# Kernel optimization log

Hardware: AMD Instinct MI355X
Metric: run time of the kernel (lower is better)

Reference implementation:

```python
import math
import jax, jax.numpy as jnp
import numpy as np

B, S, D, H = 2, 2048, 2048, 16
HD = D // H  # 128
EPS = 1e-5


def setup_inputs() -> dict:
    key = jax.random.key(0)
    ks = jax.random.split(key, 7)
    x = jax.random.normal(ks[0], (B, S, D), jnp.float32)
    # RoPE tables: (seqlen, head_dim//2)
    theta = 10000.0
    inv_freq = 1.0 / (theta ** (np.arange(0, HD, 2, dtype=np.float32) / HD))
    t = np.arange(S, dtype=np.float32)
    freqs = np.outer(t, inv_freq)  # (S, HD//2)
    freqs_cos = jnp.asarray(np.cos(freqs), jnp.float32)
    freqs_sin = jnp.asarray(np.sin(freqs), jnp.float32)
    sc = 0.02
    wq = jax.random.normal(ks[1], (D, D), jnp.float32) * sc  # stored (in, out)
    wk = jax.random.normal(ks[2], (D, D), jnp.float32) * sc
    wv = jax.random.normal(ks[3], (D, D), jnp.float32) * sc
    wu = jax.random.normal(ks[4], (D, D), jnp.float32) * sc
    wo = jax.random.normal(ks[5], (D, D), jnp.float32) * sc
    norm_w = jnp.ones((D,), jnp.float32)
    return {"x": x, "freqs_cos": freqs_cos, "freqs_sin": freqs_sin,
            "wq": wq, "wk": wk, "wv": wv, "wu": wu, "wo": wo, "norm_w": norm_w}


def _rope(t, cos, sin):
    # t: (B, S, H, HD); cos/sin: (S, HD//2)
    tr = t.reshape(t.shape[:-1] + (-1, 2))
    r, i = tr[..., 0], tr[..., 1]
    c = cos[None, :, None, :]
    s = sin[None, :, None, :]
    out_r = r * c - i * s
    out_i = r * s + i * c
    return jnp.stack([out_r, out_i], axis=-1).reshape(t.shape)


def reference(x, freqs_cos, freqs_sin, wq, wk, wv, wu, wo, norm_w):
    b, s, d = x.shape
    h = jax.nn.silu(x)  # pre-projection SiLU on the input
    q = (h @ wq).reshape(b, s, H, HD)
    k = (h @ wk).reshape(b, s, H, HD)
    v = (h @ wv).reshape(b, s, H, HD)
    u = h @ wu  # reshape->transpose->flatten in original is identity on (b,s,d)
    q = _rope(q, freqs_cos, freqs_sin)
    k = _rope(k, freqs_cos, freqs_sin)
    # scores: (b, H, s, s)
    scores = jnp.einsum('bqhd,bkhd->bhqk', q, k) / math.sqrt(HD)
    causal = jnp.tril(jnp.ones((s, s), bool))  # mask!=0 positions zeroed; silu(0)=0
    scores = jnp.where(causal[None, None], jax.nn.silu(scores), 0.0)
    out = jnp.einsum('bhqk,bkhd->bqhd', scores, v).reshape(b, s, d)
    # RMSNorm
    out = out * jax.lax.rsqrt(jnp.mean(out * out, axis=-1, keepdims=True) + EPS)
    out = out * norm_w
    out = out * u
    return out @ wo
```

## Files before the change

### kernel.cpp

```cpp
#include <hip/hip_runtime.h>
#include <hip/hip_bf16.h>
#include <cstdint>

typedef __attribute__((ext_vector_type(8))) short bf16x8;
typedef __attribute__((ext_vector_type(4))) float f32x4;
typedef unsigned short u16;

constexpr int B = 2, S = 2048, D = 2048, H = 16, HD = 128;
constexpr int M = B * S;
constexpr int NQKU = 6144;
constexpr float SCALE = 0.08838834764831845f;

static __device__ __forceinline__ float b2f(u16 u) {
    union { float f; uint32_t i; } v; v.i = ((uint32_t)u) << 16; return v.f;
}
static __device__ __forceinline__ u16 f2b(float f) {
    union { float f; uint32_t i; } v; v.f = f;
    uint32_t x = v.i;
    return (u16)((x + 0x7FFFu + ((x >> 16) & 1u)) >> 16);
}

__device__ __forceinline__ void gll16(const void* g, void* l) {
    __builtin_amdgcn_global_load_lds(
        (const __attribute__((address_space(1))) uint32_t*)g,
        (__attribute__((address_space(3))) uint32_t*)l, 16, 0, 0);
}

#define BAR() do { asm volatile("" ::: "memory"); __builtin_amdgcn_s_barrier(); \
                   asm volatile("" ::: "memory"); } while (0)

__global__ __launch_bounds__(256) void silu_cast(const float* __restrict__ x,
                                                 u16* __restrict__ h, int n) {
    int i = (blockIdx.x * 256 + threadIdx.x) * 4;
    if (i >= n) return;
    float4 v = *(const float4*)(x + i);
    ushort4 o;
    o.x = f2b(v.x / (1.f + __expf(-v.x)));
    o.y = f2b(v.y / (1.f + __expf(-v.y)));
    o.z = f2b(v.z / (1.f + __expf(-v.z)));
    o.w = f2b(v.w / (1.f + __expf(-v.w)));
    *(ushort4*)(h + i) = o;
}

__global__ __launch_bounds__(256) void wcast(const float* __restrict__ w,
                                             u16* __restrict__ wT) {
    __shared__ float t[64][65];
    int tx = threadIdx.x & 63, ty = threadIdx.x >> 6;
    int kb = blockIdx.y * 64, nb = blockIdx.x * 64;
    for (int r = ty; r < 64; r += 4)
        t[r][tx] = w[(size_t)(kb + r) * D + nb + tx];
    __syncthreads();
    for (int r = ty; r < 64; r += 4)
        wT[(size_t)(nb + r) * D + kb + tx] = f2b(t[tx][r]);
}

__global__ __launch_bounds__(512, 2)
void gemm_qkuv(const u16* __restrict__ A, const u16* __restrict__ BT,
               u16* __restrict__ qku, u16* __restrict__ vt) {
    __shared__ u16 lds[65536];
    const int tid = threadIdx.x;
    const int lane = tid & 63, wid = tid >> 6;
    const int wm = wid >> 2, wn = wid & 3;
    const int l16 = lane & 15, lq = lane >> 4;

    const int orig = blockIdx.x;
    const int swz = (orig & 7) * 64 + (orig >> 3);
    const int mt = swz & 15, nt = swz >> 4;
    const int m0 = mt * 256, n0 = nt * 256;

    const int srow = tid >> 2;
    const int ce = ((tid & 3) * 8) ^ (((tid >> 5) & 1) << 4);
    const int rdx = (lq * 16) ^ (((l16 >> 3) & 1) << 5);

    const u16* As0 = A + (size_t)(m0 + srow) * D + ce;
    const u16* Bs0 = BT + (size_t)(n0 + srow) * D + ce;

    {
        u16* dA = lds + wid * 512;
        u16* dB = lds + 16384 + wid * 512;
        gll16(As0,                    dA);
        gll16(As0 + (size_t)128 * D,  dA + 8192);
        gll16(Bs0,                    dB);
        gll16(Bs0 + (size_t)128 * D,  dB + 8192);
        gll16(As0 + 32,                    dA + 4096);
        gll16(As0 + 32 + (size_t)128 * D,  dA + 8192 + 4096);
        gll16(Bs0 + 32,                    dB + 4096);
        gll16(Bs0 + 32 + (size_t)128 * D,  dB + 8192 + 4096);
        u16* dA1 = lds + 32768 + wid * 512;
        u16* dB1 = lds + 32768 + 16384 + wid * 512;
        gll16(As0 + 64,                    dA1);
        gll16(As0 + 64 + (size_t)128 * D,  dA1 + 8192);
        gll16(Bs0 + 64,                    dB1);
        gll16(Bs0 + 64 + (size_t)128 * D,  dB1 + 8192);
    }
    asm volatile("s_waitcnt vmcnt(8)" ::: "memory");
    BAR();

    f32x4 acc[8][4] = {};
    bf16x8 a[8];
    const int rbB = (wn & 1) * 4096;

#define LOAD_A(kk)                                                            \
    _Pragma("unroll") for (int mi = 0; mi < 8; ++mi)                          \
        a[mi] = *(const bf16x8*)(Abase + (kk) * 8192 +                        \
                                 (mi * 16 + l16) * 64 + rdx);
#define LOAD_B(dst, nia, kk)                                                  \
    dst = *(const bf16x8*)(Bbase + (kk) * 8192 + rbB +                        \
                           ((nia) * 16 + l16) * 64 + rdx);
#define MFMA2(n0i, n1i)                                                       \
    __builtin_amdgcn_s_setprio(1);                                            \
    _Pragma("unroll") for (int mi = 0; mi < 8; ++mi) {                        \
        acc[mi][n0i] = __builtin_amdgcn_mfma_f32_16x16x32_bf16(a[mi], b0,     \
                            acc[mi][n0i], 0, 0, 0);                           \
        acc[mi][n1i] = __builtin_amdgcn_mfma_f32_16x16x32_bf16(a[mi], b1,     \
                            acc[mi][n1i], 0, 0, 0);                           \
    }                                                                          \
    __builtin_amdgcn_s_setprio(0);

    for (int kt = 0; kt < 32; ++kt) {
        const int buf = kt & 1;
        const char* Abase = (const char*)lds + buf * 65536 + wm * 16384;
        const char* Bbase = (const char*)lds + 32768 + buf * 65536 + (wn >> 1) * 16384;
        const bool st1 = (kt + 1) < 32;
        const bool st2 = (kt + 2) < 32;
        const u16* Asrc1 = As0 + (kt + 1) * 64;
        const u16* Bsrc1 = Bs0 + (kt + 1) * 64;
        const u16* Asrc2 = As0 + (kt + 2) * 64;
        const u16* Bsrc2 = Bs0 + (kt + 2) * 64;
        u16* dN = lds + (buf ^ 1) * 32768 + wid * 512;
        u16* dC = lds + buf * 32768 + wid * 512;
        bf16x8 b0, b1;

        LOAD_A(0);
        LOAD_B(b0, 0, 0);
        LOAD_B(b1, 1, 0);
        if (st1) { gll16(Asrc1 + 32, dN + 4096);
                   gll16(Asrc1 + 32 + (size_t)128 * D, dN + 8192 + 4096); }
        BAR();
        MFMA2(0, 1);
        BAR();
        LOAD_B(b0, 2, 0);
        LOAD_B(b1, 3, 0);
        if (st1) { gll16(Bsrc1 + 32, dN + 16384 + 4096);
                   gll16(Bsrc1 + 32 + (size_t)128 * D, dN + 16384 + 8192 + 4096); }
        BAR();
        MFMA2(2, 3);
        if (kt == 31) asm volatile("s_waitcnt vmcnt(0)" ::: "memory");
        else          asm volatile("s_waitcnt vmcnt(8)" ::: "memory");
        BAR();
        LOAD_A(1);
        LOAD_B(b0, 0, 1);
        LOAD_B(b1, 1, 1);
        if (st2) { gll16(Asrc2, dC);
                   gll16(Asrc2 + (size_t)128 * D, dC + 8192); }
        BAR();
        MFMA2(0, 1);
        BAR();
        LOAD_B(b0, 2, 1);
        LOAD_B(b1, 3, 1);
        if (st2) { gll16(Bsrc2, dC + 16384);
                   gll16(Bsrc2 + (size_t)128 * D, dC + 16384 + 8192); }
        BAR();
        MFMA2(2, 3);
        if (kt < 30)       asm volatile("s_waitcnt vmcnt(8)" ::: "memory");
        else if (kt == 30) asm volatile("s_waitcnt vmcnt(4)" ::: "memory");
        BAR();
    }
#undef LOAD_A
#undef LOAD_B
#undef MFMA2

    if (n0 >= NQKU) {
#pragma unroll
        for (int mi = 0; mi < 8; ++mi)
#pragma unroll
            for (int ni = 0; ni < 4; ++ni) {
                int c = n0 - NQKU + wn * 64 + ni * 16 + l16;
                int hh = c >> 7, d = c & 127;
                int row0 = m0 + wm * 128 + mi * 16 + lq * 4;
                int bb = row0 >> 11, s0 = row0 & 2047;
                ushort4 pk = make_ushort4(f2b(acc[mi][ni][0]), f2b(acc[mi][ni][1]),
                                          f2b(acc[mi][ni][2]), f2b(acc[mi][ni][3]));
                *(ushort4*)(vt + (((size_t)(bb * H + hh) * HD + d) * S + s0)) = pk;
            }
    } else {
#pragma unroll
        for (int mi = 0; mi < 8; ++mi)
#pragma unroll
            for (int ni = 0; ni < 4; ++ni)
#pragma unroll
                for (int r = 0; r < 4; ++r) {
                    int row = m0 + wm * 128 + mi * 16 + lq * 4 + r;
                    int col = n0 + wn * 64 + ni * 16 + l16;
                    qku[(size_t)row * NQKU + col] = f2b(acc[mi][ni][r]);
                }
    }
}

__global__ __launch_bounds__(256)
void gemm_bt_f32(const u16* __restrict__ A, const u16* __restrict__ BT,
                 float* __restrict__ out, int lda, int ldc, int Kk) {
    __shared__ u16 As[128 * 32];
    __shared__ u16 Bs[128 * 32];
    const int tid = threadIdx.x;
    const int lane = tid & 63, w = tid >> 6;
    const int wm = w >> 1, wn = w & 1;
    const int l16 = lane & 15, lq = lane >> 4;
    const int m0 = blockIdx.y * 128, n0 = blockIdx.x * 128;
    const int rs = lane >> 2;
    const int cs = (lane & 3) * 8;
    f32x4 acc[4][4] = {};

    const u16* Ab = A + (size_t)(m0 + w * 32 + rs) * lda + cs;
    const u16* Bb = BT + (size_t)(n0 + w * 32 + rs) * Kk + cs;
    u16* Al = As + w * 32 * 32;
    u16* Bl = Bs + w * 32 * 32;

    for (int k0 = 0; k0 < Kk; k0 += 32) {
        gll16(Ab + k0, Al);
        gll16(Ab + k0 + (size_t)16 * lda, Al + 16 * 32);
        gll16(Bb + k0, Bl);
        gll16(Bb + k0 + (size_t)16 * Kk, Bl + 16 * 32);
        __syncthreads();
        bf16x8 af[4], bfr[4];
#pragma unroll
        for (int mi = 0; mi < 4; mi++)
            af[mi] = *(const bf16x8*)(As + (wm * 64 + mi * 16 + l16) * 32 + lq * 8);
#pragma unroll
        for (int ni = 0; ni < 4; ni++)
            bfr[ni] = *(const bf16x8*)(Bs + (wn * 64 + ni * 16 + l16) * 32 + lq * 8);
#pragma unroll
        for (int mi = 0; mi < 4; mi++)
#pragma unroll
            for (int ni = 0; ni < 4; ni++)
                acc[mi][ni] = __builtin_amdgcn_mfma_f32_16x16x32_bf16(
                    af[mi], bfr[ni], acc[mi][ni], 0, 0, 0);
        __syncthreads();
    }
#pragma unroll
    for (int mi = 0; mi < 4; mi++)
#pragma unroll
        for (int ni = 0; ni < 4; ni++)
#pragma unroll
            for (int r = 0; r < 4; r++) {
                int row = m0 + wm * 64 + mi * 16 + lq * 4 + r;
                int col = n0 + wn * 64 + ni * 16 + l16;
                out[(size_t)row * ldc + col] = acc[mi][ni][r];
            }
}

__global__ __launch_bounds__(256)
void reformat(const u16* __restrict__ qku, const float* __restrict__ fc,
              const float* __restrict__ fs, u16* __restrict__ qr,
              u16* __restrict__ kr) {
    int bh = blockIdx.x;
    int s0 = blockIdx.y * 64;
    int b = bh >> 4, h = bh & 15;
    int tid = threadIdx.x;
#pragma unroll
    for (int i = 0; i < 16; ++i) {
        int p = tid + i * 256;
        int row = p >> 6, pp = p & 63;
        int sgl = s0 + row;
        float c = fc[sgl * 64 + pp], sn = fs[sgl * 64 + pp];
        size_t src = (size_t)(b * S + sgl) * NQKU + h * HD + 2 * pp;
        size_t dst = ((size_t)bh * S + sgl) * HD + 2 * pp;
        {
            uint32_t qv = *(const uint32_t*)(qku + src);
            float r = b2f((u16)(qv & 0xffff)), im = b2f((u16)(qv >> 16));
            uint32_t o = (uint32_t)f2b(r * c - im * sn) |
                         ((uint32_t)f2b(r * sn + im * c) << 16);
            *(uint32_t*)(qr + dst) = o;
        }
        {
            uint32_t kv = *(const uint32_t*)(qku + src + 2048);
            float r = b2f((u16)(kv & 0xffff)), im = b2f((u16)(kv >> 16));
            uint32_t o = (uint32_t)f2b(r * c - im * sn) |
                         ((uint32_t)f2b(r * sn + im * c) << 16);
            *(uint32_t*)(kr + dst) = o;
        }
    }
}

__global__ __launch_bounds__(512, 2)
void hstu_attn(const u16* __restrict__ qr, const u16* __restrict__ kr,
               const u16* __restrict__ vt, u16* __restrict__ attb) {
    __shared__ u16 k_l[16384];
    __shared__ u16 v_l[16384];
    __shared__ u16 s_l[128 * 136];
    const int id = blockIdx.x;
    const int bh = (id & 7) * 4 + ((id >> 3) & 3);
    const int slot = id >> 5;
    const int b = bh >> 4, h = bh & 15;
    const int tid = threadIdx.x, lane = tid & 63, w = tid >> 6;
    const int l16 = lane & 15, lq = lane >> 4;
    const int wq = w >> 2, wk4 = w & 3;

    const u16* kb = kr + (size_t)bh * S * HD;
    const u16* vb = vt + (size_t)bh * HD * S;
    const int irow0 = tid >> 4, iu0 = tid & 15;

#define STAGE_K(k0_)                                                          \
    _Pragma("unroll") for (int r_ = 0; r_ < 4; ++r_) {                        \
        int row_ = irow0 + r_ * 32;                                           \
        int uc_ = iu0 ^ (row_ & 7);                                           \
        gll16(kb + (size_t)(k0_ + row_) * HD + uc_ * 8,                       \
              k_l + ((w * 64 + r_ * 512) << 3));                              \
    }
#define STAGE_V(k0_)                                                          \
    _Pragma("unroll") for (int r_ = 0; r_ < 4; ++r_) {                        \
        int row_ = irow0 + r_ * 32;                                           \
        int uc_ = iu0 ^ (row_ & 7);                                           \
        gll16(vb + (size_t)row_ * S + (k0_) + uc_ * 8,                        \
              v_l + ((w * 64 + r_ * 512) << 3));                              \
    }

    for (int pass = 0; pass < 2; ++pass) {
        const int t = pass ? (15 - slot) : slot;
        const int q0 = t * 128;

        bf16x8 qf[4][4];
#pragma unroll
        for (int mi = 0; mi < 4; ++mi)
#pragma unroll
            for (int kk = 0; kk < 4; ++kk)
                qf[mi][kk] = *(const bf16x8*)(qr +
                    ((size_t)bh * S + q0 + wq * 64 + mi * 16 + l16) * HD +
                    kk * 32 + lq * 8);
        f32x4 acco[4][2] = {};

        STAGE_K(0);
        STAGE_V(0);
        asm volatile("s_waitcnt vmcnt(0)" ::: "memory");
        BAR();

        for (int kt = 0; kt <= t; ++kt) {
            const int k0 = kt * 128;
            const bool st = kt < t;
            f32x4 accs[4][2] = {};
            __builtin_amdgcn_s_setprio(1);
#pragma unroll
            for (int kk = 0; kk < 4; ++kk)
#pragma unroll
                for (int ni = 0; ni < 2; ++ni) {
                    int row = wk4 * 32 + ni * 16 + l16;
                    bf16x8 kf = *(const bf16x8*)(k_l + row * 128 +
                                ((kk * 32 + lq * 8) ^ ((row & 7) << 3)));
#pragma unroll
                    for (int mi = 0; mi < 4; ++mi)
                        accs[mi][ni] = __builtin_amdgcn_mfma_f32_16x16x32_bf16(
                            qf[mi][kk], kf, accs[mi][ni], 0, 0, 0);
                }
            __builtin_amdgcn_s_setprio(0);
            const bool dg = (kt == t);
#pragma unroll
            for (int mi = 0; mi < 4; ++mi)
#pragma unroll
                for (int ni = 0; ni < 2; ++ni)
#pragma unroll
                    for (int r = 0; r < 4; ++r) {
                        int qrow = wq * 64 + mi * 16 + lq * 4 + r;
                        int krow = wk4 * 32 + ni * 16 + l16;
                        float vv = accs[mi][ni][r] * SCALE;
                        vv = (!dg || (k0 + krow <= q0 + qrow))
                                 ? vv * __builtin_amdgcn_rcpf(1.f + __expf(-vv))
                                 : 0.f;
                        s_l[qrow * 136 + krow] = f2b(vv);
                    }
            BAR();
            if (st) STAGE_K(k0 + 128);
            if (st) asm volatile("s_waitcnt vmcnt(4)" ::: "memory");
            else    asm volatile("s_waitcnt vmcnt(0)" ::: "memory");
            BAR();
            __builtin_amdgcn_s_setprio(1);
#pragma unroll
            for (int kk = 0; kk < 4; ++kk) {
                bf16x8 sf[4];
#pragma unroll
                for (int mi = 0; mi < 4; ++mi)
                    sf[mi] = *(const bf16x8*)(s_l + (wq * 64 + mi * 16 + l16) * 136 +
                                              kk * 32 + lq * 8);
#pragma unroll
                for (int ni = 0; ni < 2; ++ni) {
                    int row = wk4 * 32 + ni * 16 + l16;
                    bf16x8 vf = *(const bf16x8*)(v_l + row * 128 +
                                ((kk * 32 + lq * 8) ^ ((row & 7) << 3)));
#pragma unroll
                    for (int mi = 0; mi < 4; ++mi)
                        acco[mi][ni] = __builtin_amdgcn_mfma_f32_16x16x32_bf16(
                            sf[mi], vf, acco[mi][ni], 0, 0, 0);
                }
            }
            __builtin_amdgcn_s_setprio(0);
            BAR();
            if (st) {
                STAGE_V(k0 + 128);
                asm volatile("s_waitcnt vmcnt(4)" ::: "memory");
            }
            BAR();
        }
#pragma unroll
        for (int mi = 0; mi < 4; ++mi)
#pragma unroll
            for (int ni = 0; ni < 2; ++ni)
#pragma unroll
                for (int r = 0; r < 4; ++r)
                    attb[(size_t)(b * S + q0 + wq * 64 + mi * 16 + lq * 4 + r) * NQKU +
                         h * HD + wk4 * 32 + ni * 16 + l16] = f2b(acco[mi][ni][r]);
    }
#undef STAGE_K
#undef STAGE_V
}

__global__ __launch_bounds__(256)
void rms_mul(u16* __restrict__ qku, const float* __restrict__ nw) {
    int row = blockIdx.x;
    int tid = threadIdx.x;
    int col = tid * 8;
    u16 at[8];
    *(int4*)at = *(const int4*)(qku + (size_t)row * NQKU + col);
    float f[8];
    float ss = 0.f;
#pragma unroll
    for (int j = 0; j < 8; j++) { f[j] = b2f(at[j]); ss += f[j] * f[j]; }
#pragma unroll
    for (int off = 32; off > 0; off >>= 1) ss += __shfl_down(ss, off, 64);
    __shared__ float red[4];
    int lane = tid & 63, w = tid >> 6;
    if (lane == 0) red[w] = ss;
    __syncthreads();
    float rs = rsqrtf((red[0] + red[1] + red[2] + red[3]) * (1.f / D) + 1e-5f);
    u16* up = qku + (size_t)row * NQKU + 4096 + col;
    u16 ut[8];
    *(int4*)ut = *(const int4*)up;
    u16 o[8];
#pragma unroll
    for (int j = 0; j < 8; j++)
        o[j] = f2b(f[j] * rs * nw[col + j] * b2f(ut[j]));
    *(int4*)up = *(int4*)o;
}

extern "C" void kernel_launch(void* const* d_in, const int* in_sizes, int n_in,
                              void* d_out, int out_size, void* d_ws, size_t ws_size,
                              hipStream_t stream) {
    const float* x  = (const float*)d_in[0];
    const float* fc = (const float*)d_in[1];
    const float* fs = (const float*)d_in[2];
    const float* wq = (const float*)d_in[3];
    const float* wk = (const float*)d_in[4];
    const float* wv = (const float*)d_in[5];
    const float* wu = (const float*)d_in[6];
    const float* wo = (const float*)d_in[7];
    const float* nw = (const float*)d_in[8];
    float* out = (float*)d_out;

    char* ws = (char*)d_ws;
    const size_t WSZ = (size_t)D * D * sizeof(u16);
    u16* h_b  = (u16*)(ws);
    u16* wT   = (u16*)(ws + 2 * WSZ);
    u16* qku  = (u16*)(ws + 7 * WSZ);
    u16* vt   = (u16*)(ws + 13 * WSZ);
    u16* k_r  = (u16*)(ws + 15 * WSZ);
    u16* q_r  = h_b;

    silu_cast<<<M * D / 1024, 256, 0, stream>>>(x, h_b, M * D);
    dim3 wg(32, 32);
    wcast<<<wg, 256, 0, stream>>>(wq, wT + 0 * (size_t)D * D);
    wcast<<<wg, 256, 0, stream>>>(wk, wT + 1 * (size_t)D * D);
    wcast<<<wg, 256, 0, stream>>>(wu, wT + 2 * (size_t)D * D);
    wcast<<<wg, 256, 0, stream>>>(wv, wT + 3 * (size_t)D * D);
    wcast<<<wg, 256, 0, stream>>>(wo, wT + 4 * (size_t)D * D);

    gemm_qkuv<<<512, 512, 0, stream>>>(h_b, wT, qku, vt);

    reformat<<<dim3(32, 32), 256, 0, stream>>>(qku, fc, fs, q_r, k_r);
    hstu_attn<<<256, 512, 0, stream>>>(q_r, k_r, vt, qku);
    rms_mul<<<M, 256, 0, stream>>>(qku, nw);
    gemm_bt_f32<<<dim3(D / 128, M / 128), 256, 0, stream>>>(
        qku + 4096, wT + 4 * (size_t)D * D, out, NQKU, D, D);
}
```

Measured before the change: 340.9 us.

## Double-buffer 64-key attention tiles and merge five weight-cast launches

```diff
diff --git a/kernel.cpp b/kernel.cpp
--- a/kernel.cpp
+++ b/kernel.cpp
@@ -42,16 +42,21 @@
     *(ushort4*)(h + i) = o;
 }
 
-__global__ __launch_bounds__(256) void wcast(const float* __restrict__ w,
-                                             u16* __restrict__ wT) {
+__global__ __launch_bounds__(256)
+void wcast5(const float* __restrict__ w0, const float* __restrict__ w1,
+            const float* __restrict__ w2, const float* __restrict__ w3,
+            const float* __restrict__ w4, u16* __restrict__ wT) {
     __shared__ float t[64][65];
+    int z = blockIdx.z;
+    const float* w = (z == 0) ? w0 : (z == 1) ? w1 : (z == 2) ? w2 : (z == 3) ? w3 : w4;
+    u16* dst = wT + (size_t)z * D * D;
     int tx = threadIdx.x & 63, ty = threadIdx.x >> 6;
     int kb = blockIdx.y * 64, nb = blockIdx.x * 64;
     for (int r = ty; r < 64; r += 4)
         t[r][tx] = w[(size_t)(kb + r) * D + nb + tx];
     __syncthreads();
     for (int r = ty; r < 64; r += 4)
-        wT[(size_t)(nb + r) * D + kb + tx] = f2b(t[tx][r]);
+        dst[(size_t)(nb + r) * D + kb + tx] = f2b(t[tx][r]);
 }
 
 __global__ __launch_bounds__(512, 2)
@@ -282,12 +287,12 @@
     }
 }
 
-__global__ __launch_bounds__(512, 2)
+__global__ __launch_bounds__(512, 1)
 void hstu_attn(const u16* __restrict__ qr, const u16* __restrict__ kr,
                const u16* __restrict__ vt, u16* __restrict__ attb) {
-    __shared__ u16 k_l[16384];
-    __shared__ u16 v_l[16384];
-    __shared__ u16 s_l[128 * 136];
+    __shared__ u16 k_l[2 * 8192];
+    __shared__ u16 v_l[2 * 8192];
+    __shared__ u16 s_l[128 * 72];
     const int id = blockIdx.x;
     const int bh = (id & 7) * 4 + ((id >> 3) & 3);
     const int slot = id >> 5;
@@ -298,93 +303,97 @@
 
     const u16* kb = kr + (size_t)bh * S * HD;
     const u16* vb = vt + (size_t)bh * HD * S;
-    const int irow0 = tid >> 4, iu0 = tid & 15;
-
-#define STAGE_K(k0_)                                                          \
-    _Pragma("unroll") for (int r_ = 0; r_ < 4; ++r_) {                        \
-        int row_ = irow0 + r_ * 32;                                           \
-        int uc_ = iu0 ^ (row_ & 7);                                           \
-        gll16(kb + (size_t)(k0_ + row_) * HD + uc_ * 8,                       \
-              k_l + ((w * 64 + r_ * 512) << 3));                              \
-    }
-#define STAGE_V(k0_)                                                          \
-    _Pragma("unroll") for (int r_ = 0; r_ < 4; ++r_) {                        \
-        int row_ = irow0 + r_ * 32;                                           \
-        int uc_ = iu0 ^ (row_ & 7);                                           \
-        gll16(vb + (size_t)row_ * S + (k0_) + uc_ * 8,                        \
-              v_l + ((w * 64 + r_ * 512) << 3));                              \
-    }
+    const u16* qb = qr + (size_t)bh * S * HD;
+
+#define STAGE_K(k0_, bf_) do {                                                \
+    _Pragma("unroll") for (int r_ = 0; r_ < 2; ++r_) {                        \
+        int i_ = tid + r_ * 512;                                              \
+        int row_ = i_ >> 4, iu_ = i_ & 15;                                    \
+        int uc_ = iu_ ^ (row_ & 7);                                           \
+        gll16(kb + (size_t)((k0_) + row_) * HD + uc_ * 8,                     \
+              k_l + (bf_) * 8192 + ((w * 64 + r_ * 512) << 3));               \
+    } } while (0)
+#define STAGE_V(k0_, bf_) do {                                                \
+    _Pragma("unroll") for (int r_ = 0; r_ < 2; ++r_) {                        \
+        int i_ = tid + r_ * 512;                                              \
+        int d_ = i_ >> 3, iu_ = i_ & 7;                                       \
+        int uc_ = iu_ ^ (d_ & 7);                                             \
+        gll16(vb + (size_t)d_ * S + (k0_) + uc_ * 8,                          \
+              v_l + (bf_) * 8192 + ((w * 64 + r_ * 512) << 3));               \
+    } } while (0)
 
     for (int pass = 0; pass < 2; ++pass) {
-        const int t = pass ? (15 - slot) : slot;
-        const int q0 = t * 128;
+        const int tq = pass ? (15 - slot) : slot;
+        const int q0 = tq * 128;
+        const int kmax = 2 * tq + 1;
 
         bf16x8 qf[4][4];
 #pragma unroll
         for (int mi = 0; mi < 4; ++mi)
 #pragma unroll
             for (int kk = 0; kk < 4; ++kk)
-                qf[mi][kk] = *(const bf16x8*)(qr +
-                    ((size_t)bh * S + q0 + wq * 64 + mi * 16 + l16) * HD +
-                    kk * 32 + lq * 8);
+                qf[mi][kk] = *(const bf16x8*)(qb +
+                    (size_t)(q0 + wq * 64 + mi * 16 + l16) * HD + kk * 32 + lq * 8);
         f32x4 acco[4][2] = {};
 
-        STAGE_K(0);
-        STAGE_V(0);
-        asm volatile("s_waitcnt vmcnt(0)" ::: "memory");
-        BAR();
-
-        for (int kt = 0; kt <= t; ++kt) {
-            const int k0 = kt * 128;
-            const bool st = kt < t;
-            f32x4 accs[4][2] = {};
+        STAGE_K(0, 0);
+        STAGE_V(0, 0);
+        STAGE_K(64, 1);
+        STAGE_V(64, 1);
+        asm volatile("s_waitcnt vmcnt(8)" ::: "memory");
+        BAR();
+
+        for (int kt = 0; kt <= kmax; ++kt) {
+            const int k0 = kt * 64;
+            const int buf = kt & 1;
+            f32x4 accs[4] = {};
             __builtin_amdgcn_s_setprio(1);
 #pragma unroll
-            for (int kk = 0; kk < 4; ++kk)
+            for (int kk = 0; kk < 4; ++kk) {
+                int row = wk4 * 16 + l16;
+                bf16x8 kf = *(const bf16x8*)(k_l + buf * 8192 + row * 128 +
+                            ((kk * 32 + lq * 8) ^ ((row & 7) << 3)));
+#pragma unroll
+                for (int mi = 0; mi < 4; ++mi)
+                    accs[mi] = __builtin_amdgcn_mfma_f32_16x16x32_bf16(
+                        qf[mi][kk], kf, accs[mi], 0, 0, 0);
+            }
+            __builtin_amdgcn_s_setprio(0);
+            const bool dg = (kt >= 2 * tq);
+#pragma unroll
+            for (int mi = 0; mi < 4; ++mi)
+#pragma unroll
+                for (int r = 0; r < 4; ++r) {
+                    int qrow = wq * 64 + mi * 16 + lq * 4 + r;
+                    int krow = wk4 * 16 + l16;
+                    float vv = accs[mi][r] * SCALE;
+                    vv = (!dg || (k0 + krow <= q0 + qrow))
+                             ? vv * __builtin_amdgcn_rcpf(1.f + __expf(-vv))
+                             : 0.f;
+                    s_l[qrow * 72 + krow] = f2b(vv);
+                }
+            BAR();
+            if (kt + 2 <= kmax) STAGE_K((kt + 2) * 64, buf);
+            if (kt <= kmax - 2)
+                asm volatile("s_waitcnt vmcnt(12)" ::: "memory");
+            else if (kt == kmax - 1)
+                asm volatile("s_waitcnt vmcnt(8)" ::: "memory");
+            else
+                asm volatile("s_waitcnt vmcnt(0)" ::: "memory");
+            BAR();
+            __builtin_amdgcn_s_setprio(1);
+#pragma unroll
+            for (int kk = 0; kk < 2; ++kk) {
+                bf16x8 sf[4];
+#pragma unroll
+                for (int mi = 0; mi < 4; ++mi)
+                    sf[mi] = *(const bf16x8*)(s_l + (wq * 64 + mi * 16 + l16) * 72 +
+                                              kk * 32 + lq * 8);
 #pragma unroll
                 for (int ni = 0; ni < 2; ++ni) {
                     int row = wk4 * 32 + ni * 16 + l16;
-                    bf16x8 kf = *(const bf16x8*)(k_l + row * 128 +
-                                ((kk * 32 + lq * 8) ^ ((row & 7) << 3)));
-#pragma unroll
-                    for (int mi = 0; mi < 4; ++mi)
-                        accs[mi][ni] = __builtin_amdgcn_mfma_f32_16x16x32_bf16(
-                            qf[mi][kk], kf, accs[mi][ni], 0, 0, 0);
-                }
-            __builtin_amdgcn_s_setprio(0);
-            const bool dg = (kt == t);
-#pragma unroll
-            for (int mi = 0; mi < 4; ++mi)
-#pragma unroll
-                for (int ni = 0; ni < 2; ++ni)
-#pragma unroll
-                    for (int r = 0; r < 4; ++r) {
-                        int qrow = wq * 64 + mi * 16 + lq * 4 + r;
-                        int krow = wk4 * 32 + ni * 16 + l16;
-                        float vv = accs[mi][ni][r] * SCALE;
-                        vv = (!dg || (k0 + krow <= q0 + qrow))
-                                 ? vv * __builtin_amdgcn_rcpf(1.f + __expf(-vv))
-                                 : 0.f;
-                        s_l[qrow * 136 + krow] = f2b(vv);
-                    }
-            BAR();
-            if (st) STAGE_K(k0 + 128);
-            if (st) asm volatile("s_waitcnt vmcnt(4)" ::: "memory");
-            else    asm volatile("s_waitcnt vmcnt(0)" ::: "memory");
-            BAR();
-            __builtin_amdgcn_s_setprio(1);
-#pragma unroll
-            for (int kk = 0; kk < 4; ++kk) {
-                bf16x8 sf[4];
-#pragma unroll
-                for (int mi = 0; mi < 4; ++mi)
-                    sf[mi] = *(const bf16x8*)(s_l + (wq * 64 + mi * 16 + l16) * 136 +
-                                              kk * 32 + lq * 8);
-#pragma unroll
-                for (int ni = 0; ni < 2; ++ni) {
-                    int row = wk4 * 32 + ni * 16 + l16;
-                    bf16x8 vf = *(const bf16x8*)(v_l + row * 128 +
-                                ((kk * 32 + lq * 8) ^ ((row & 7) << 3)));
+                    bf16x8 vf = *(const bf16x8*)(v_l + buf * 8192 + row * 64 +
+                                (((kk * 4 + lq) ^ (row & 7)) << 3));
 #pragma unroll
                     for (int mi = 0; mi < 4; ++mi)
                         acco[mi][ni] = __builtin_amdgcn_mfma_f32_16x16x32_bf16(
@@ -393,10 +402,11 @@
             }
             __builtin_amdgcn_s_setprio(0);
             BAR();
-            if (st) {
-                STAGE_V(k0 + 128);
+            if (kt + 2 <= kmax) STAGE_V((kt + 2) * 64, buf);
+            if (kt <= kmax - 2)
+                asm volatile("s_waitcnt vmcnt(12)" ::: "memory");
+            else if (kt == kmax - 1)
                 asm volatile("s_waitcnt vmcnt(4)" ::: "memory");
-            }
             BAR();
         }
 #pragma unroll
@@ -464,12 +474,7 @@
     u16* q_r  = h_b;
 
     silu_cast<<<M * D / 1024, 256, 0, stream>>>(x, h_b, M * D);
-    dim3 wg(32, 32);
-    wcast<<<wg, 256, 0, stream>>>(wq, wT + 0 * (size_t)D * D);
-    wcast<<<wg, 256, 0, stream>>>(wk, wT + 1 * (size_t)D * D);
-    wcast<<<wg, 256, 0, stream>>>(wu, wT + 2 * (size_t)D * D);
-    wcast<<<wg, 256, 0, stream>>>(wv, wT + 3 * (size_t)D * D);
-    wcast<<<wg, 256, 0, stream>>>(wo, wT + 4 * (size_t)D * D);
+    wcast5<<<dim3(32, 32, 5), 256, 0, stream>>>(wq, wk, wu, wv, wo, wT);
 
     gemm_qkuv<<<512, 512, 0, stream>>>(h_b, wT, qku, vt);
 
```

Measured after the change: 329.4 us. 1.03x faster.
